# Performance work log

Measured on AMD Instinct MI355X. Metric: run time of the kernel, lower is better.

Reference implementation:

```python
import jax, jax.numpy as jnp
import numpy as np

D_MODEL = 1024
NUM_HEADS = 16
D_HEAD = D_MODEL // NUM_HEADS
B, T_Q, T_K = 2, 2048, 2048


def setup_inputs() -> dict:
    key = jax.random.key(0)
    ks = jax.random.split(key, 7)
    s = 0.02
    return {
        "query": jax.random.normal(ks[0], (B, T_Q, D_MODEL), jnp.float32),
        "key_value": jax.random.normal(ks[1], (B, T_K, D_MODEL), jnp.float32),
        "mask": jax.random.randint(ks[2], (B, 1, T_Q, T_K), 0, 2, jnp.int32),
        "rel_pos_bias": jax.random.normal(ks[3], (NUM_HEADS, T_Q, T_K), jnp.float32),
        "Wq": jax.random.normal(ks[4], (D_MODEL, D_MODEL), jnp.float32) * s,
        "Wkv": jax.random.normal(ks[5], (D_MODEL, 2 * D_MODEL), jnp.float32) * s,
        "Wo": jax.random.normal(ks[6], (D_MODEL, D_MODEL), jnp.float32) * s,
    }


def reference(query, key_value, mask, rel_pos_bias, Wq, Wkv, Wo):
    Bq, Tq, D = query.shape
    Tk = key_value.shape[1]
    H, Dh = NUM_HEADS, D_HEAD
    q = (query @ Wq).reshape(Bq, Tq, H, Dh)              # [B,Tq,H,Dh]
    kv = (key_value @ Wkv).reshape(Bq, Tk, 2, H, Dh)
    k, v = kv[:, :, 0], kv[:, :, 1]                      # [B,Tk,H,Dh]
    scale = 1.0 / jnp.sqrt(jnp.asarray(Dh, q.dtype))
    scores = jnp.einsum("bqhd,bkhd->bhqk", q, k) * scale  # [B,H,Tq,Tk]
    scores = scores + rel_pos_bias[None]                  # bias broadcast over batch
    scores = jnp.where(mask == 0, -jnp.inf, scores)
    attn = jax.nn.softmax(scores, axis=-1)
    out = jnp.einsum("bhqk,bkhd->bqhd", attn, v).reshape(Bq, Tq, D)
    return out @ Wo
```

## Files before the change

kernel.cpp:

```cpp
#include <hip/hip_runtime.h>

typedef unsigned short u16;
typedef unsigned int u32;
typedef unsigned long long u64;
typedef __attribute__((ext_vector_type(4))) float f32x4;
typedef __attribute__((ext_vector_type(4))) unsigned short u16x4;
typedef __attribute__((ext_vector_type(4))) short s16x4;
typedef __attribute__((ext_vector_type(8))) short short8;

#define GLOAD16(G, L) __builtin_amdgcn_global_load_lds( \
    (const __attribute__((address_space(1))) void*)(G), \
    (__attribute__((address_space(3))) void*)(L), 16, 0, 0)

__device__ __forceinline__ u16 f2bf(float f) {
  union { float f; unsigned u; } c; c.f = f;
  unsigned u = c.u;
  u += 0x7FFFu + ((u >> 16) & 1u);
  return (u16)(u >> 16);
}

__device__ __forceinline__ void store_out(u16* p, float v) { *p = f2bf(v); }
__device__ __forceinline__ void store_out(float* p, float v) { *p = v; }

__global__ void k_cvt(const float* __restrict__ in, u16* __restrict__ out, int n4) {
  int i = blockIdx.x * blockDim.x + threadIdx.x;
  if (i >= n4) return;
  const f32x4 v = *(const f32x4*)(in + (size_t)i * 4);
  u16x4 o;
  o[0] = f2bf(v[0]); o[1] = f2bf(v[1]); o[2] = f2bf(v[2]); o[3] = f2bf(v[3]);
  *(u16x4*)(out + (size_t)i * 4) = o;
}

__global__ void k_tcvt(const float* __restrict__ src, u16* __restrict__ dst,
                       int R, int C, float scale) {
  __shared__ float t[32][33];
  int bx = blockIdx.x * 32;
  int by = blockIdx.y * 32;
  int tx = threadIdx.x, ty = threadIdx.y;
  #pragma unroll
  for (int j = 0; j < 32; j += 8)
    t[ty + j][tx] = src[(size_t)(by + ty + j) * C + bx + tx];
  __syncthreads();
  #pragma unroll
  for (int j = 0; j < 32; j += 8)
    dst[(size_t)(bx + ty + j) * R + by + tx] = f2bf(t[tx][ty + j] * scale);
}

__global__ void k_tv(const u16* __restrict__ kv, u16* __restrict__ vt) {
  __shared__ u16 t[32][34];
  int b = blockIdx.z;
  int tb = blockIdx.x * 32;
  int db = blockIdx.y * 32;
  int tx = threadIdx.x, ty = threadIdx.y;
  #pragma unroll
  for (int j = 0; j < 32; j += 8)
    t[ty + j][tx] = kv[(size_t)(b * 2048 + tb + ty + j) * 2048 + 1024 + db + tx];
  __syncthreads();
  #pragma unroll
  for (int j = 0; j < 32; j += 8)
    vt[(size_t)(b * 1024 + db + ty + j) * 2048 + tb + tx] = t[tx][ty + j];
}

__global__ void k_pm(const int* __restrict__ mask, unsigned* __restrict__ bits, int nw) {
  int w = blockIdx.x * blockDim.x + threadIdx.x;
  if (w >= nw) return;
  const int4* p = (const int4*)(mask + (size_t)w * 32);
  unsigned b = 0;
  #pragma unroll
  for (int j = 0; j < 8; ++j) {
    int4 v = p[j];
    b |= (v.x != 0 ? 1u : 0u) << (j * 4);
    b |= (v.y != 0 ? 1u : 0u) << (j * 4 + 1);
    b |= (v.z != 0 ? 1u : 0u) << (j * 4 + 2);
    b |= (v.w != 0 ? 1u : 0u) << (j * 4 + 3);
  }
  bits[w] = b;
}

template <typename OUT_T>
__global__ __launch_bounds__(256) void k_gemm(
    const u16* __restrict__ A, const u16* __restrict__ Bt,
    OUT_T* __restrict__ C, int M, int N, int K)
{
  __shared__ u16 As[128 * 64];
  __shared__ u16 Bs[128 * 64];
  const int tid = threadIdx.x;
  const int lane = tid & 63;
  const int w = tid >> 6;
  const int wr = w >> 1, wc = w & 1;
  const int l16 = lane & 15, lh = lane >> 4;
  const size_t tm = blockIdx.x, tn = blockIdx.y;

  f32x4 acc[4][4] = {};

  for (int kt = 0; kt < K; kt += 64) {
    #pragma unroll
    for (int i = 0; i < 4; ++i) {
      int flat = i * 256 + tid;
      int row = flat >> 3, cb = flat & 7;
      GLOAD16(A + (tm * 128 + row) * K + kt + ((cb ^ (row & 7)) * 8),
              (char*)As + flat * 16);
    }
    #pragma unroll
    for (int i = 0; i < 4; ++i) {
      int flat = i * 256 + tid;
      int row = flat >> 3, cb = flat & 7;
      GLOAD16(Bt + (tn * 128 + row) * K + kt + ((cb ^ (row & 7)) * 8),
              (char*)Bs + flat * 16);
    }
    __syncthreads();
    #pragma unroll
    for (int kk = 0; kk < 2; ++kk) {
      short8 a[4], b[4];
      #pragma unroll
      for (int mi = 0; mi < 4; ++mi) {
        int row = wr * 64 + mi * 16 + l16;
        a[mi] = *(const short8*)&As[row * 64 + ((kk * 32 + lh * 8) ^ ((row & 7) * 8))];
      }
      #pragma unroll
      for (int ni = 0; ni < 4; ++ni) {
        int row = wc * 64 + ni * 16 + l16;
        b[ni] = *(const short8*)&Bs[row * 64 + ((kk * 32 + lh * 8) ^ ((row & 7) * 8))];
      }
      #pragma unroll
      for (int mi = 0; mi < 4; ++mi)
        #pragma unroll
        for (int ni = 0; ni < 4; ++ni)
          acc[mi][ni] = __builtin_amdgcn_mfma_f32_16x16x32_bf16(a[mi], b[ni], acc[mi][ni], 0, 0, 0);
    }
    __syncthreads();
  }
  #pragma unroll
  for (int mi = 0; mi < 4; ++mi)
    #pragma unroll
    for (int ni = 0; ni < 4; ++ni)
      #pragma unroll
      for (int r = 0; r < 4; ++r) {
        size_t row = tm * 128 + wr * 64 + mi * 16 + lh * 4 + r;
        size_t col = tn * 128 + wc * 64 + ni * 16 + l16;
        store_out(&C[row * N + col], acc[mi][ni][r]);
      }
}

__global__ __launch_bounds__(512, 4) void k_attn(
    const u16* __restrict__ Qp,
    const u16* __restrict__ KVp,
    const u16* __restrict__ Vt,
    const float* __restrict__ bias,
    const unsigned* __restrict__ mbits,
    u16* __restrict__ Ob)
{
  __shared__ u16 Ks[2 * 2 * 64 * 64];
  __shared__ u16 Vs[2 * 2 * 64 * 64];
  const int tid = threadIdx.x;
  const int lane = tid & 63;
  const int w = tid >> 6;
  const int bw = w >> 2;
  const int qs = (w & 3) * 16;
  const int qt = blockIdx.x;
  const int h  = blockIdx.y;
  const int l16 = lane & 15, lh = lane >> 4;
  const int q = qt * 64 + qs + l16;

  const int srow = tid >> 3, scb = tid & 7;
  const u16* ksrc = KVp + (size_t)srow * 2048 + h * 64 + ((scb ^ (srow & 7)) * 8);
  const u16* vsrc = Vt + ((size_t)(h * 64 + srow)) * 2048 + (((2 * scb) ^ (srow & 14)) * 4);

  short8 qf[2];
  {
    size_t row = (size_t)bw * 2048 + q;
    qf[0] = *(const short8*)&Qp[row * 1024 + h * 64 + lh * 8];
    qf[1] = *(const short8*)&Qp[row * 1024 + h * 64 + 32 + lh * 8];
  }

  const float* bsrc = bias + ((size_t)h * 2048 + q) * 2048 + lh * 4;
  const u64*   msrc = (const u64*)(mbits + ((size_t)bw * 2048 + q) * 64);

  f32x4 oacc[4] = {};
  float lpart = 0.f;

  GLOAD16(ksrc + (size_t)(0 * 2048) * 2048, &Ks[0 * 8192 + 0 * 4096 + tid * 8]);
  GLOAD16(ksrc + (size_t)(1 * 2048 + 0) * 2048, &Ks[0 * 8192 + 1 * 4096 + tid * 8]);
  GLOAD16(vsrc + (size_t)(0 * 1024) * 2048, &Vs[0 * 8192 + 0 * 4096 + tid * 8]);
  GLOAD16(vsrc + (size_t)(1 * 1024) * 2048, &Vs[0 * 8192 + 1 * 4096 + tid * 8]);

  f32x4 bias_cur[4];
  #pragma unroll
  for (int ni = 0; ni < 4; ++ni)
    bias_cur[ni] = *(const f32x4*)(bsrc + 0 * 64 + ni * 16);
  u64 mw_cur = msrc[0];

  asm volatile("s_waitcnt vmcnt(0)" ::: "memory");
  __builtin_amdgcn_s_barrier();

  for (int kt = 0; kt < 32; ++kt) {
    const int cur = kt & 1;

    f32x4 bias_nxt[4];
    u64 mw_nxt;
    if (kt + 1 < 32) {
      const int nb = cur ^ 1;
      const size_t kro = (size_t)((kt + 1) * 64) * 2048;
      const size_t vco = (size_t)((kt + 1) * 64);
      GLOAD16(ksrc + (size_t)(0 * 2048) * 2048 + kro, &Ks[nb * 8192 + 0 * 4096 + tid * 8]);
      GLOAD16(ksrc + (size_t)(1 * 2048) * 2048 + kro, &Ks[nb * 8192 + 1 * 4096 + tid * 8]);
      GLOAD16(vsrc + (size_t)(0 * 1024) * 2048 + vco, &Vs[nb * 8192 + 0 * 4096 + tid * 8]);
      GLOAD16(vsrc + (size_t)(1 * 1024) * 2048 + vco, &Vs[nb * 8192 + 1 * 4096 + tid * 8]);
      #pragma unroll
      for (int ni = 0; ni < 4; ++ni)
        bias_nxt[ni] = *(const f32x4*)(bsrc + (size_t)(kt + 1) * 64 + ni * 16);
      mw_nxt = msrc[kt + 1];
    }

    f32x4 s[4];
    #pragma unroll
    for (int ni = 0; ni < 4; ++ni) s[ni] = bias_cur[ni];
    const int kbase = cur * 8192 + bw * 4096;
    #pragma unroll
    for (int kk = 0; kk < 2; ++kk) {
      short8 kf[4];
      #pragma unroll
      for (int ni = 0; ni < 4; ++ni) {
        int row = ni * 16 + l16;
        kf[ni] = *(const short8*)&Ks[kbase + row * 64 + ((kk * 32 + lh * 8) ^ ((row & 7) * 8))];
      }
      #pragma unroll
      for (int ni = 0; ni < 4; ++ni)
        s[ni] = __builtin_amdgcn_mfma_f32_16x16x32_bf16(kf[ni], qf[kk], s[ni], 0, 0, 0);
    }

    u32 pb[4][2];
    {
      unsigned tlo = (unsigned)(mw_cur) >> (lh * 4);
      unsigned thi = (unsigned)(mw_cur >> 32) >> (lh * 4);
      #pragma unroll
      for (int ni = 0; ni < 4; ++ni) {
        unsigned tw = (ni < 2) ? tlo : thi;
        #pragma unroll
        for (int r = 0; r < 4; ++r) {
          unsigned bit = (tw >> ((ni & 1) * 16 + r)) & 1u;
          float pv = bit ? __expf(s[ni][r]) : 0.f;
          lpart += pv;
          s[ni][r] = pv;
        }
        asm("v_cvt_pk_bf16_f32 %0, %1, %2" : "=v"(pb[ni][0]) : "v"(s[ni][0]), "v"(s[ni][1]));
        asm("v_cvt_pk_bf16_f32 %0, %1, %2" : "=v"(pb[ni][1]) : "v"(s[ni][2]), "v"(s[ni][3]));
      }
    }

    const int vbase = cur * 8192 + bw * 4096;
    #pragma unroll
    for (int kk = 0; kk < 2; ++kk) {
      union { u32 w[4]; short8 v; } pf;
      pf.w[0] = pb[2 * kk][0];
      pf.w[1] = pb[2 * kk][1];
      pf.w[2] = pb[2 * kk + 1][0];
      pf.w[3] = pb[2 * kk + 1][1];
      #pragma unroll
      for (int di = 0; di < 4; ++di) {
        int row = di * 16 + l16;
        int sw = row & 14;
        s16x4 v0 = *(const s16x4*)&Vs[vbase + row * 64 + (((8 * kk + lh) ^ sw) * 4)];
        s16x4 v1 = *(const s16x4*)&Vs[vbase + row * 64 + (((8 * kk + 4 + lh) ^ sw) * 4)];
        short8 vf = __builtin_shufflevector(v0, v1, 0, 1, 2, 3, 4, 5, 6, 7);
        oacc[di] = __builtin_amdgcn_mfma_f32_16x16x32_bf16(vf, pf.v, oacc[di], 0, 0, 0);
      }
    }

    #pragma unroll
    for (int ni = 0; ni < 4; ++ni) bias_cur[ni] = bias_nxt[ni];
    mw_cur = mw_nxt;

    asm volatile("s_waitcnt vmcnt(0)" ::: "memory");
    __builtin_amdgcn_s_barrier();
  }

  lpart += __shfl_xor(lpart, 16);
  lpart += __shfl_xor(lpart, 32);
  float inv = 1.0f / lpart;
  size_t orow = (size_t)bw * 2048 + q;
  #pragma unroll
  for (int di = 0; di < 4; ++di)
    #pragma unroll
    for (int rp = 0; rp < 2; ++rp) {
      float v0 = oacc[di][2 * rp] * inv;
      float v1 = oacc[di][2 * rp + 1] * inv;
      u32 pk;
      asm("v_cvt_pk_bf16_f32 %0, %1, %2" : "=v"(pk) : "v"(v0), "v"(v1));
      *(u32*)&Ob[orow * 1024 + h * 64 + di * 16 + lh * 4 + rp * 2] = pk;
    }
}

extern "C" void kernel_launch(void* const* d_in, const int* in_sizes, int n_in,
                              void* d_out, int out_size, void* d_ws, size_t ws_size,
                              hipStream_t stream) {
  const float* query     = (const float*)d_in[0];
  const float* key_value = (const float*)d_in[1];
  const int*   mask      = (const int*)d_in[2];
  const float* bias      = (const float*)d_in[3];
  const float* Wq        = (const float*)d_in[4];
  const float* Wkv       = (const float*)d_in[5];
  const float* Wo        = (const float*)d_in[6];
  float* out = (float*)d_out;

  char* ws = (char*)d_ws;
  u16* qb   = (u16*)(ws);
  u16* kvb  = (u16*)(ws + 8388608);
  u16* WqT  = (u16*)(ws + 16777216);
  u16* WkvT = (u16*)(ws + 18874368);
  u16* WoT  = (u16*)(ws + 23068672);
  u16* Qp   = (u16*)(ws + 25165824);
  u16* KVp  = (u16*)(ws + 33554432);
  u16* Vt   = (u16*)(ws + 50331648);
  u16* Ob   = (u16*)(ws + 58720256);
  unsigned* mb = (unsigned*)(ws + 67108864);

  dim3 tb(32, 8);
  k_cvt<<<4096, 256, 0, stream>>>(query, qb, 1048576);
  k_cvt<<<4096, 256, 0, stream>>>(key_value, kvb, 1048576);
  k_tcvt<<<dim3(32, 32), tb, 0, stream>>>(Wq,  WqT,  1024, 1024, 0.125f);
  k_tcvt<<<dim3(64, 32), tb, 0, stream>>>(Wkv, WkvT, 1024, 2048, 1.0f);
  k_tcvt<<<dim3(32, 32), tb, 0, stream>>>(Wo,  WoT,  1024, 1024, 1.0f);
  k_pm<<<1024, 256, 0, stream>>>(mask, mb, 262144);
  k_gemm<u16><<<dim3(32, 8),  256, 0, stream>>>(qb,  WqT,  Qp,  4096, 1024, 1024);
  k_gemm<u16><<<dim3(32, 16), 256, 0, stream>>>(kvb, WkvT, KVp, 4096, 2048, 1024);
  k_tv<<<dim3(64, 32, 2), tb, 0, stream>>>(KVp, Vt);
  k_attn<<<dim3(32, 16), 512, 0, stream>>>(Qp, KVp, Vt, bias, mb, Ob);
  k_gemm<float><<<dim3(32, 8), 256, 0, stream>>>(Ob, WoT, out, 4096, 1024, 1024);
}
```

Baseline: 250.5 us.

## Permute V transpose layout, unroll attention loop by two, shrink GEMM tiles

The V-transpose kernel now writes keys in a permuted column order, so the attention kernel can load each V fragment as one 16-byte LDS read with the same XOR swizzle used for K. The attention loop is unrolled by two with ping-pong bias and mask registers. It issues next-tile loads unconditionally (clamped at the last tile), waits with vmcnt(5) instead of a full drain, and accumulates the row sum in a vector. The GEMMs are templated on tile size and launched with 64x128 tiles, giving twice as many blocks for better CU occupancy at the cost of less reuse per block.

```diff
diff --git a/kernel.cpp b/kernel.cpp
--- a/kernel.cpp
+++ b/kernel.cpp
@@ -5,7 +5,6 @@
 typedef unsigned long long u64;
 typedef __attribute__((ext_vector_type(4))) float f32x4;
 typedef __attribute__((ext_vector_type(4))) unsigned short u16x4;
-typedef __attribute__((ext_vector_type(4))) short s16x4;
 typedef __attribute__((ext_vector_type(8))) short short8;
 
 #define GLOAD16(G, L) __builtin_amdgcn_global_load_lds( \
@@ -47,18 +46,21 @@
 }
 
 __global__ void k_tv(const u16* __restrict__ kv, u16* __restrict__ vt) {
-  __shared__ u16 t[32][34];
+  __shared__ u16 sh[32][34];
   int b = blockIdx.z;
   int tb = blockIdx.x * 32;
   int db = blockIdx.y * 32;
   int tx = threadIdx.x, ty = threadIdx.y;
   #pragma unroll
   for (int j = 0; j < 32; j += 8)
-    t[ty + j][tx] = kv[(size_t)(b * 2048 + tb + ty + j) * 2048 + 1024 + db + tx];
+    sh[ty + j][tx] = kv[(size_t)(b * 2048 + tb + ty + j) * 2048 + 1024 + db + tx];
   __syncthreads();
+  int t = tb + tx;
+  int k6 = t & 63;
+  int colp = (t & ~63) | (((k6 >> 2) & 3) << 4) | ((k6 >> 4) << 2) | (k6 & 3);
   #pragma unroll
   for (int j = 0; j < 32; j += 8)
-    vt[(size_t)(b * 1024 + db + ty + j) * 2048 + tb + tx] = t[tx][ty + j];
+    vt[(size_t)(b * 1024 + db + ty + j) * 2048 + colp] = sh[tx][ty + j];
 }
 
 __global__ void k_pm(const int* __restrict__ mask, unsigned* __restrict__ bits, int nw) {
@@ -77,13 +79,14 @@
   bits[w] = b;
 }
 
-template <typename OUT_T>
+template <int BM, int BN, typename OUT_T>
 __global__ __launch_bounds__(256) void k_gemm(
     const u16* __restrict__ A, const u16* __restrict__ Bt,
     OUT_T* __restrict__ C, int M, int N, int K)
 {
-  __shared__ u16 As[128 * 64];
-  __shared__ u16 Bs[128 * 64];
+  constexpr int MI = BM / 32, NI = BN / 32;
+  __shared__ u16 As[BM * 64];
+  __shared__ u16 Bs[BN * 64];
   const int tid = threadIdx.x;
   const int lane = tid & 63;
   const int w = tid >> 6;
@@ -91,53 +94,53 @@
   const int l16 = lane & 15, lh = lane >> 4;
   const size_t tm = blockIdx.x, tn = blockIdx.y;
 
-  f32x4 acc[4][4] = {};
+  f32x4 acc[MI][NI] = {};
 
   for (int kt = 0; kt < K; kt += 64) {
     #pragma unroll
-    for (int i = 0; i < 4; ++i) {
+    for (int i = 0; i < BM / 32; ++i) {
       int flat = i * 256 + tid;
       int row = flat >> 3, cb = flat & 7;
-      GLOAD16(A + (tm * 128 + row) * K + kt + ((cb ^ (row & 7)) * 8),
+      GLOAD16(A + (tm * BM + row) * K + kt + ((cb ^ (row & 7)) * 8),
               (char*)As + flat * 16);
     }
     #pragma unroll
-    for (int i = 0; i < 4; ++i) {
+    for (int i = 0; i < BN / 32; ++i) {
       int flat = i * 256 + tid;
       int row = flat >> 3, cb = flat & 7;
-      GLOAD16(Bt + (tn * 128 + row) * K + kt + ((cb ^ (row & 7)) * 8),
+      GLOAD16(Bt + (tn * BN + row) * K + kt + ((cb ^ (row & 7)) * 8),
               (char*)Bs + flat * 16);
     }
     __syncthreads();
     #pragma unroll
     for (int kk = 0; kk < 2; ++kk) {
-      short8 a[4], b[4];
+      short8 a[MI], b[NI];
       #pragma unroll
-      for (int mi = 0; mi < 4; ++mi) {
-        int row = wr * 64 + mi * 16 + l16;
+      for (int mi = 0; mi < MI; ++mi) {
+        int row = wr * (BM / 2) + mi * 16 + l16;
         a[mi] = *(const short8*)&As[row * 64 + ((kk * 32 + lh * 8) ^ ((row & 7) * 8))];
       }
       #pragma unroll
-      for (int ni = 0; ni < 4; ++ni) {
-        int row = wc * 64 + ni * 16 + l16;
+      for (int ni = 0; ni < NI; ++ni) {
+        int row = wc * (BN / 2) + ni * 16 + l16;
         b[ni] = *(const short8*)&Bs[row * 64 + ((kk * 32 + lh * 8) ^ ((row & 7) * 8))];
       }
       #pragma unroll
-      for (int mi = 0; mi < 4; ++mi)
+      for (int mi = 0; mi < MI; ++mi)
         #pragma unroll
-        for (int ni = 0; ni < 4; ++ni)
+        for (int ni = 0; ni < NI; ++ni)
           acc[mi][ni] = __builtin_amdgcn_mfma_f32_16x16x32_bf16(a[mi], b[ni], acc[mi][ni], 0, 0, 0);
     }
     __syncthreads();
   }
   #pragma unroll
-  for (int mi = 0; mi < 4; ++mi)
-    #pragma unroll
-    for (int ni = 0; ni < 4; ++ni)
+  for (int mi = 0; mi < MI; ++mi)
+    #pragma unroll
+    for (int ni = 0; ni < NI; ++ni)
       #pragma unroll
       for (int r = 0; r < 4; ++r) {
-        size_t row = tm * 128 + wr * 64 + mi * 16 + lh * 4 + r;
-        size_t col = tn * 128 + wc * 64 + ni * 16 + l16;
+        size_t row = tm * BM + wr * (BM / 2) + mi * 16 + lh * 4 + r;
+        size_t col = tn * BN + wc * (BN / 2) + ni * 16 + l16;
         store_out(&C[row * N + col], acc[mi][ni][r]);
       }
 }
@@ -164,7 +167,7 @@
 
   const int srow = tid >> 3, scb = tid & 7;
   const u16* ksrc = KVp + (size_t)srow * 2048 + h * 64 + ((scb ^ (srow & 7)) * 8);
-  const u16* vsrc = Vt + ((size_t)(h * 64 + srow)) * 2048 + (((2 * scb) ^ (srow & 14)) * 4);
+  const u16* vsrc = Vt + ((size_t)(h * 64 + srow)) * 2048 + ((scb ^ (srow & 7)) * 8);
 
   short8 qf[2];
   {
@@ -177,104 +180,87 @@
   const u64*   msrc = (const u64*)(mbits + ((size_t)bw * 2048 + q) * 64);
 
   f32x4 oacc[4] = {};
-  float lpart = 0.f;
-
-  GLOAD16(ksrc + (size_t)(0 * 2048) * 2048, &Ks[0 * 8192 + 0 * 4096 + tid * 8]);
-  GLOAD16(ksrc + (size_t)(1 * 2048 + 0) * 2048, &Ks[0 * 8192 + 1 * 4096 + tid * 8]);
-  GLOAD16(vsrc + (size_t)(0 * 1024) * 2048, &Vs[0 * 8192 + 0 * 4096 + tid * 8]);
-  GLOAD16(vsrc + (size_t)(1 * 1024) * 2048, &Vs[0 * 8192 + 1 * 4096 + tid * 8]);
-
-  f32x4 bias_cur[4];
-  #pragma unroll
-  for (int ni = 0; ni < 4; ++ni)
-    bias_cur[ni] = *(const f32x4*)(bsrc + 0 * 64 + ni * 16);
-  u64 mw_cur = msrc[0];
-
+  f32x4 lpv = {};
+  f32x4 biasA[4], biasB[4];
+  u64 mwA, mwB;
+
+  GLOAD16(ksrc,                       &Ks[tid * 8]);
+  GLOAD16(ksrc + (size_t)2048 * 2048, &Ks[4096 + tid * 8]);
+  GLOAD16(vsrc,                       &Vs[tid * 8]);
+  GLOAD16(vsrc + (size_t)1024 * 2048, &Vs[4096 + tid * 8]);
+  biasA[0] = *(const f32x4*)(bsrc +  0);
+  biasA[1] = *(const f32x4*)(bsrc + 16);
+  biasA[2] = *(const f32x4*)(bsrc + 32);
+  biasA[3] = *(const f32x4*)(bsrc + 48);
+  mwA = msrc[0];
   asm volatile("s_waitcnt vmcnt(0)" ::: "memory");
   __builtin_amdgcn_s_barrier();
 
-  for (int kt = 0; kt < 32; ++kt) {
-    const int cur = kt & 1;
-
-    f32x4 bias_nxt[4];
-    u64 mw_nxt;
-    if (kt + 1 < 32) {
-      const int nb = cur ^ 1;
-      const size_t kro = (size_t)((kt + 1) * 64) * 2048;
-      const size_t vco = (size_t)((kt + 1) * 64);
-      GLOAD16(ksrc + (size_t)(0 * 2048) * 2048 + kro, &Ks[nb * 8192 + 0 * 4096 + tid * 8]);
-      GLOAD16(ksrc + (size_t)(1 * 2048) * 2048 + kro, &Ks[nb * 8192 + 1 * 4096 + tid * 8]);
-      GLOAD16(vsrc + (size_t)(0 * 1024) * 2048 + vco, &Vs[nb * 8192 + 0 * 4096 + tid * 8]);
-      GLOAD16(vsrc + (size_t)(1 * 1024) * 2048 + vco, &Vs[nb * 8192 + 1 * 4096 + tid * 8]);
-      #pragma unroll
-      for (int ni = 0; ni < 4; ++ni)
-        bias_nxt[ni] = *(const f32x4*)(bsrc + (size_t)(kt + 1) * 64 + ni * 16);
-      mw_nxt = msrc[kt + 1];
-    }
-
-    f32x4 s[4];
-    #pragma unroll
-    for (int ni = 0; ni < 4; ++ni) s[ni] = bias_cur[ni];
-    const int kbase = cur * 8192 + bw * 4096;
-    #pragma unroll
-    for (int kk = 0; kk < 2; ++kk) {
-      short8 kf[4];
-      #pragma unroll
-      for (int ni = 0; ni < 4; ++ni) {
-        int row = ni * 16 + l16;
-        kf[ni] = *(const short8*)&Ks[kbase + row * 64 + ((kk * 32 + lh * 8) ^ ((row & 7) * 8))];
-      }
-      #pragma unroll
-      for (int ni = 0; ni < 4; ++ni)
-        s[ni] = __builtin_amdgcn_mfma_f32_16x16x32_bf16(kf[ni], qf[kk], s[ni], 0, 0, 0);
-    }
-
-    u32 pb[4][2];
-    {
-      unsigned tlo = (unsigned)(mw_cur) >> (lh * 4);
-      unsigned thi = (unsigned)(mw_cur >> 32) >> (lh * 4);
-      #pragma unroll
-      for (int ni = 0; ni < 4; ++ni) {
-        unsigned tw = (ni < 2) ? tlo : thi;
-        #pragma unroll
-        for (int r = 0; r < 4; ++r) {
-          unsigned bit = (tw >> ((ni & 1) * 16 + r)) & 1u;
-          float pv = bit ? __expf(s[ni][r]) : 0.f;
-          lpart += pv;
-          s[ni][r] = pv;
-        }
-        asm("v_cvt_pk_bf16_f32 %0, %1, %2" : "=v"(pb[ni][0]) : "v"(s[ni][0]), "v"(s[ni][1]));
-        asm("v_cvt_pk_bf16_f32 %0, %1, %2" : "=v"(pb[ni][1]) : "v"(s[ni][2]), "v"(s[ni][3]));
-      }
-    }
-
-    const int vbase = cur * 8192 + bw * 4096;
-    #pragma unroll
-    for (int kk = 0; kk < 2; ++kk) {
-      union { u32 w[4]; short8 v; } pf;
-      pf.w[0] = pb[2 * kk][0];
-      pf.w[1] = pb[2 * kk][1];
-      pf.w[2] = pb[2 * kk + 1][0];
-      pf.w[3] = pb[2 * kk + 1][1];
-      #pragma unroll
-      for (int di = 0; di < 4; ++di) {
-        int row = di * 16 + l16;
-        int sw = row & 14;
-        s16x4 v0 = *(const s16x4*)&Vs[vbase + row * 64 + (((8 * kk + lh) ^ sw) * 4)];
-        s16x4 v1 = *(const s16x4*)&Vs[vbase + row * 64 + (((8 * kk + 4 + lh) ^ sw) * 4)];
-        short8 vf = __builtin_shufflevector(v0, v1, 0, 1, 2, 3, 4, 5, 6, 7);
-        oacc[di] = __builtin_amdgcn_mfma_f32_16x16x32_bf16(vf, pf.v, oacc[di], 0, 0, 0);
-      }
-    }
-
-    #pragma unroll
-    for (int ni = 0; ni < 4; ++ni) bias_cur[ni] = bias_nxt[ni];
-    mw_cur = mw_nxt;
-
-    asm volatile("s_waitcnt vmcnt(0)" ::: "memory");
-    __builtin_amdgcn_s_barrier();
+#define ASTEP(KT, CUR, BC, MC, BN_, MN_) do {                                            \
+    const int ktn_ = ((KT) + 1 < 32) ? (KT) + 1 : 31;                                    \
+    GLOAD16(ksrc + (size_t)ktn_ * 64 * 2048,                  &Ks[((CUR)^1) * 8192 + tid * 8]);        \
+    GLOAD16(ksrc + ((size_t)2048 + (size_t)ktn_ * 64) * 2048, &Ks[((CUR)^1) * 8192 + 4096 + tid * 8]); \
+    GLOAD16(vsrc + (size_t)ktn_ * 64,                         &Vs[((CUR)^1) * 8192 + tid * 8]);        \
+    GLOAD16(vsrc + (size_t)1024 * 2048 + (size_t)ktn_ * 64,   &Vs[((CUR)^1) * 8192 + 4096 + tid * 8]); \
+    __builtin_amdgcn_sched_barrier(0);                                                   \
+    f32x4 s_[4];                                                                         \
+    s_[0] = BC[0]; s_[1] = BC[1]; s_[2] = BC[2]; s_[3] = BC[3];                          \
+    const unsigned tlo_ = (unsigned)(MC) >> (lh * 4);                                    \
+    const unsigned thi_ = (unsigned)((MC) >> 32) >> (lh * 4);                            \
+    BN_[0] = *(const f32x4*)(bsrc + (size_t)ktn_ * 64 +  0);                             \
+    BN_[1] = *(const f32x4*)(bsrc + (size_t)ktn_ * 64 + 16);                             \
+    BN_[2] = *(const f32x4*)(bsrc + (size_t)ktn_ * 64 + 32);                             \
+    BN_[3] = *(const f32x4*)(bsrc + (size_t)ktn_ * 64 + 48);                             \
+    MN_ = msrc[ktn_];                                                                    \
+    const int kb_ = (CUR) * 8192 + bw * 4096;                                            \
+    _Pragma("unroll")                                                                    \
+    for (int kk = 0; kk < 2; ++kk) {                                                     \
+      short8 kf_[4];                                                                     \
+      _Pragma("unroll")                                                                  \
+      for (int ni = 0; ni < 4; ++ni) {                                                   \
+        const int row_ = ni * 16 + l16;                                                  \
+        kf_[ni] = *(const short8*)&Ks[kb_ + row_ * 64 + ((kk * 32 + lh * 8) ^ ((row_ & 7) * 8))]; \
+      }                                                                                  \
+      _Pragma("unroll")                                                                  \
+      for (int ni = 0; ni < 4; ++ni)                                                     \
+        s_[ni] = __builtin_amdgcn_mfma_f32_16x16x32_bf16(kf_[ni], qf[kk], s_[ni], 0, 0, 0); \
+    }                                                                                    \
+    _Pragma("unroll")                                                                    \
+    for (int kk = 0; kk < 2; ++kk) {                                                     \
+      union { u32 wd[4]; short8 v; } pf_;                                                \
+      _Pragma("unroll")                                                                  \
+      for (int half = 0; half < 2; ++half) {                                             \
+        const int ni = 2 * kk + half;                                                    \
+        const unsigned tw_ = (ni < 2) ? tlo_ : thi_;                                     \
+        _Pragma("unroll")                                                                \
+        for (int r = 0; r < 4; ++r) {                                                    \
+          const unsigned bit_ = (tw_ >> ((ni & 1) * 16 + r)) & 1u;                       \
+          float pv_ = bit_ ? __expf(s_[ni][r]) : 0.f;                                    \
+          s_[ni][r] = pv_;                                                               \
+        }                                                                                \
+        lpv += s_[ni];                                                                   \
+        asm("v_cvt_pk_bf16_f32 %0, %1, %2" : "=v"(pf_.wd[2*half])   : "v"(s_[ni][0]), "v"(s_[ni][1])); \
+        asm("v_cvt_pk_bf16_f32 %0, %1, %2" : "=v"(pf_.wd[2*half+1]) : "v"(s_[ni][2]), "v"(s_[ni][3])); \
+      }                                                                                  \
+      _Pragma("unroll")                                                                  \
+      for (int di = 0; di < 4; ++di) {                                                   \
+        const int row_ = di * 16 + l16;                                                  \
+        short8 vf_ = *(const short8*)&Vs[kb_ + row_ * 64 + (((lh * 2 + kk) * 8) ^ ((row_ & 7) * 8))]; \
+        oacc[di] = __builtin_amdgcn_mfma_f32_16x16x32_bf16(vf_, pf_.v, oacc[di], 0, 0, 0); \
+      }                                                                                  \
+    }                                                                                    \
+    asm volatile("s_waitcnt lgkmcnt(0)" ::: "memory");                                   \
+    asm volatile("s_waitcnt vmcnt(5)" ::: "memory");                                     \
+    __builtin_amdgcn_s_barrier();                                                        \
+  } while (0)
+
+  for (int kt2 = 0; kt2 < 32; kt2 += 2) {
+    ASTEP(kt2,     0, biasA, mwA, biasB, mwB);
+    ASTEP(kt2 + 1, 1, biasB, mwB, biasA, mwA);
   }
-
+#undef ASTEP
+
+  float lpart = lpv[0] + lpv[1] + lpv[2] + lpv[3];
   lpart += __shfl_xor(lpart, 16);
   lpart += __shfl_xor(lpart, 32);
   float inv = 1.0f / lpart;
@@ -322,9 +308,9 @@
   k_tcvt<<<dim3(64, 32), tb, 0, stream>>>(Wkv, WkvT, 1024, 2048, 1.0f);
   k_tcvt<<<dim3(32, 32), tb, 0, stream>>>(Wo,  WoT,  1024, 1024, 1.0f);
   k_pm<<<1024, 256, 0, stream>>>(mask, mb, 262144);
-  k_gemm<u16><<<dim3(32, 8),  256, 0, stream>>>(qb,  WqT,  Qp,  4096, 1024, 1024);
-  k_gemm<u16><<<dim3(32, 16), 256, 0, stream>>>(kvb, WkvT, KVp, 4096, 2048, 1024);
+  k_gemm<64, 128, u16><<<dim3(64, 8),  256, 0, stream>>>(qb,  WqT,  Qp,  4096, 1024, 1024);
+  k_gemm<64, 128, u16><<<dim3(64, 16), 256, 0, stream>>>(kvb, WkvT, KVp, 4096, 2048, 1024);
   k_tv<<<dim3(64, 32, 2), tb, 0, stream>>>(KVp, Vt);
   k_attn<<<dim3(32, 16), 512, 0, stream>>>(Qp, KVp, Vt, bias, mb, Ob);
-  k_gemm<float><<<dim3(32, 8), 256, 0, stream>>>(Ob, WoT, out, 4096, 1024, 1024);
-}
+  k_gemm<64, 128, float><<<dim3(64, 8), 256, 0, stream>>>(Ob, WoT, out, 4096, 1024, 1024);
+}
```

After: 223.1 us. -10.9%, faster.
